# Kernel tuning notes

Measured on AMD Instinct MI355X. Metric: run time of the kernel, lower is better.

Reference implementation:

```python
import jax, jax.numpy as jnp
import numpy as np
from jax import lax

SEQ, BSZ = 64, 32
NTOK, NINP, NHID, NLAYERS = 50000, 512, 1024, 2
BN_EPS = 1e-5


def setup_inputs() -> dict:
    key = jax.random.key(0)
    ks = jax.random.split(key, 12)
    s = 0.05
    return {
        "input_ids": jax.random.randint(ks[0], (SEQ, BSZ), 0, NTOK),
        "hx": jnp.zeros((NLAYERS, BSZ, NHID), jnp.float32),
        "cx": jnp.zeros((NLAYERS, BSZ, NHID), jnp.float32),
        "emb_w": jax.random.normal(ks[1], (NTOK, NINP), jnp.float32) * 0.01,
        "Wih0": jax.random.normal(ks[2], (4 * NHID, NINP), jnp.float32) * s,
        "Whh0": jax.random.normal(ks[3], (4 * NHID, NHID), jnp.float32) * s,
        "bih0": jnp.zeros((4 * NHID,), jnp.float32),
        "bhh0": jnp.zeros((4 * NHID,), jnp.float32),
        "Wih1": jax.random.normal(ks[4], (4 * NHID, NHID), jnp.float32) * s,
        "Whh1": jax.random.normal(ks[5], (4 * NHID, NHID), jnp.float32) * s,
        "bih1": jnp.zeros((4 * NHID,), jnp.float32),
        "bhh1": jnp.zeros((4 * NHID,), jnp.float32),
        "Wp": jax.random.normal(ks[6], (NINP, NHID), jnp.float32) * s,
        "bp": jnp.zeros((NINP,), jnp.float32),
        "Wd": jax.random.normal(ks[7], (NTOK, NINP), jnp.float32) * 0.01,
        "bd": jnp.zeros((NTOK,), jnp.float32),
    }


def _lstm_cell(x, h, c, Wih, Whh, bih, bhh):
    # torch.nn.LSTMCell math; gates packed as [i, f, g, o]
    gates = x @ Wih.T + bih + h @ Whh.T + bhh  # [B, 4H]
    i, f, g, o = jnp.split(gates, 4, axis=-1)
    i = jax.nn.sigmoid(i)
    f = jax.nn.sigmoid(f)
    g = jnp.tanh(g)
    o = jax.nn.sigmoid(o)
    c2 = f * c + i * g
    h2 = o * jnp.tanh(c2)
    return h2, c2


def reference(input_ids, hx, cx, emb_w, Wih0, Whh0, bih0, bhh0,
              Wih1, Whh1, bih1, bhh1, Wp, bp, Wd, bd):
    # eval mode: drop / internal_drop / rdrop are identity; rmask == 1
    emb = emb_w[input_ids]  # [S, B, ninp]
    layers = ((Wih0, Whh0, bih0, bhh0), (Wih1, Whh1, bih1, bhh1))

    def step(carry, x_t):
        h, c = carry  # each [nlayers, B, H]
        hi = x_t
        hs, cs = [], []
        for j in range(NLAYERS):
            Wih, Whh, bih, bhh = layers[j]
            hj, cj = _lstm_cell(hi, h[j], c[j], Wih, Whh, bih, bhh)
            hs.append(hj)
            cs.append(cj)
            hi = hj
        return (jnp.stack(hs, 0), jnp.stack(cs, 0)), hi

    (hxf, cxf), out = lax.scan(step, (hx, cx), emb)  # out: [S, B, H]
    flat = out.reshape(-1, NHID)  # [S*B, H]
    # predictor: Linear -> BatchNorm1d (eval: running_mean=0, running_var=1,
    # gamma=1, beta=0) -> Tanh
    pre = flat @ Wp.T + bp
    p = jnp.tanh(pre * (1.0 / jnp.sqrt(jnp.float32(1.0 + BN_EPS))))
    decoded = p @ Wd.T + bd  # [S*B, ntoken]
    return decoded.reshape(SEQ, BSZ, NTOK), (hxf, cxf)
```

## Files before the change

### kernel.cpp

```cpp
#include <hip/hip_runtime.h>
#include <hip/hip_bf16.h>

using bf16 = __hip_bfloat16;
typedef __attribute__((ext_vector_type(8))) short short8;
typedef __attribute__((ext_vector_type(4))) float f32x4;

#define MFMA_BF16(A,B,C) __builtin_amdgcn_mfma_f32_16x16x32_bf16((A),(B),(C),0,0,0)

static __device__ __forceinline__ unsigned bf16bits(float f) {
  union { bf16 h; unsigned short u; } cv; cv.h = __float2bfloat16(f); return cv.u;
}

static __device__ __forceinline__ void gload16(const void* g, void* l) {
  __builtin_amdgcn_global_load_lds(
      (const __attribute__((address_space(1))) void*)g,
      (__attribute__((address_space(3))) void*)l, 16, 0, 0);
}

template<int EPI>
__global__ __launch_bounds__(256)
void gemm_bt(const bf16* __restrict__ A, const bf16* __restrict__ B,
             const float* __restrict__ bias1, const float* __restrict__ bias2,
             float* __restrict__ Cf, bf16* __restrict__ Cb,
             int M, int N, int K, int Nreal)
{
  __shared__ __align__(1024) bf16 As[128*32];
  __shared__ __align__(1024) bf16 Bs[128*32];
  const int tid  = threadIdx.x;
  const int wave = tid >> 6, lane = tid & 63;
  const int wr = wave >> 1, wc = wave & 1;
  const int row0 = blockIdx.y * 128;
  const int col0 = blockIdx.x * 128;

  f32x4 acc[4][4];
  #pragma unroll
  for (int m = 0; m < 4; ++m)
    #pragma unroll
    for (int n = 0; n < 4; ++n) { f32x4 z = {0.f,0.f,0.f,0.f}; acc[m][n] = z; }

  const int r_sub = lane >> 2;
  const int kc    = lane & 3;

  for (int k0 = 0; k0 < K; k0 += 32) {
    __syncthreads();
    #pragma unroll
    for (int j = 0; j < 2; ++j) {
      const int rb = wave*32 + j*16;
      gload16(A + (size_t)(row0 + rb + r_sub)*K + k0 + kc*8,
              (void*)((char*)As + (size_t)rb*64));
      gload16(B + (size_t)(col0 + rb + r_sub)*K + k0 + kc*8,
              (void*)((char*)Bs + (size_t)rb*64));
    }
    __syncthreads();

    short8 af[4], bfv[4];
    #pragma unroll
    for (int m = 0; m < 4; ++m)
      af[m] = *(const short8*)(As + (wr*64 + m*16 + (lane&15))*32 + (lane>>4)*8);
    #pragma unroll
    for (int n = 0; n < 4; ++n)
      bfv[n] = *(const short8*)(Bs + (wc*64 + n*16 + (lane&15))*32 + (lane>>4)*8);
    #pragma unroll
    for (int m = 0; m < 4; ++m)
      #pragma unroll
      for (int n = 0; n < 4; ++n)
        acc[m][n] = MFMA_BF16(af[m], bfv[n], acc[m][n]);
  }

  const float BN_SCALE = 0.9999950000374997f;
  #pragma unroll
  for (int m = 0; m < 4; ++m) {
    const int rg0 = row0 + wr*64 + m*16 + ((lane>>4)<<2);
    #pragma unroll
    for (int n = 0; n < 4; ++n) {
      const int cg = col0 + wc*64 + n*16 + (lane&15);
      if (EPI == 2) {
        const int bq = cg >> 4, q = cg & 15;
        const int orig = (q>>2)*1024 + bq*4 + (q&3);
        const float bb = bias1[orig] + bias2[orig];
        #pragma unroll
        for (int j = 0; j < 4; ++j) {
          const int row = rg0 + j;
          Cf[((size_t)bq*64 + (row>>5))*512 + (size_t)(row&31)*16 + q]
              = acc[m][n][j] + bb;
        }
      } else if (cg < Nreal) {
        float bb = 0.f;
        if (bias1) bb += bias1[cg];
        if (bias2) bb += bias2[cg];
        #pragma unroll
        for (int j = 0; j < 4; ++j) {
          float v = acc[m][n][j] + bb;
          if (EPI == 1) {
            v = tanhf(v * BN_SCALE);
            Cb[(size_t)(rg0+j)*Nreal + cg] = __float2bfloat16(v);
          } else {
            Cf[(size_t)(rg0+j)*Nreal + cg] = v;
          }
        }
      }
    }
  }
}

__global__ __launch_bounds__(256, 1)
void k_lstm_persist(const bf16* __restrict__ hinit, const float* __restrict__ cx,
                    const bf16* __restrict__ Wpack, const float* __restrict__ g0p,
                    const float* __restrict__ bih1, const float* __restrict__ bhh1,
                    bf16* __restrict__ h0_all, bf16* __restrict__ h1_all,
                    float* __restrict__ tail, unsigned* __restrict__ flags)
{
  const int b    = blockIdx.x;
  const int tid  = threadIdx.x;
  const int wave = tid >> 6, lane = tid & 63;

  __shared__ __align__(1024) bf16 Wlds[96*512];
  __shared__ float P[4][2][32][20];

  const bf16* wbase = Wpack + (size_t)b * 96 * 512;
  #pragma unroll
  for (int it = 0; it < 24; ++it) {
    const int chunk = it*4 + wave;
    gload16(wbase + (size_t)chunk*512 + lane*8,
            (void*)((char*)Wlds + (size_t)chunk*1024));
  }

  const int layer = tid >> 7;
  const int cell  = tid & 127;
  const int r     = cell >> 2;
  const int hc    = cell & 3;
  const int col   = b*4 + hc;
  float creg = cx[(size_t)layer*32768 + (size_t)r*1024 + col];
  float bsum[4];
  #pragma unroll
  for (int g = 0; g < 4; ++g)
    bsum[g] = (layer == 1) ? (bih1[g*1024 + col] + bhh1[g*1024 + col]) : 0.f;

  const int arow = lane & 15;
  const int koff = (lane >> 4) * 8;

  const unsigned* fp0 = flags + (lane*4+0)*32;
  const unsigned* fp1 = flags + (lane*4+1)*32;
  const unsigned* fp2 = flags + (lane*4+2)*32;
  const unsigned* fp3 = flags + (lane*4+3)*32;

  __syncthreads();

  for (int s = 0; s < 65; ++s) {
    const bf16* hA = (s == 0) ? hinit           : h0_all + (size_t)(s-1)*32768;
    const bf16* hB = (s <= 1) ? (hinit + 32768) : h1_all + (size_t)(s-2)*32768;

    short8 a0[8], a1[8], c0[8], c1[8];
    #pragma unroll
    for (int i = 0; i < 8; ++i) {
      const int kb = wave*256 + i*32 + koff;
      a0[i] = *(const short8*)(hA + (size_t)arow*1024      + kb);
      a1[i] = *(const short8*)(hA + (size_t)(arow+16)*1024 + kb);
      c0[i] = *(const short8*)(hB + (size_t)arow*1024      + kb);
      c1[i] = *(const short8*)(hB + (size_t)(arow+16)*1024 + kb);
    }
    float gpre[4] = {0.f, 0.f, 0.f, 0.f};
    if (layer == 0 && s < 64) {
      const float* gr = g0p + ((size_t)(b*64 + s)*32 + r)*16;
      #pragma unroll
      for (int g = 0; g < 4; ++g) gpre[g] = gr[g*4 + hc];
    }

    f32x4 z = {0.f,0.f,0.f,0.f};
    f32x4 acc00 = z, acc01 = z, acc10 = z, acc11 = z;
    #pragma unroll
    for (int i = 0; i < 8; ++i) {
      const int ks = wave*8 + i;
      short8 w0 = *(const short8*)(Wlds + ((size_t)(     ks)*64 + lane)*8);
      short8 w1 = *(const short8*)(Wlds + ((size_t)(32 + ks)*64 + lane)*8);
      short8 w2 = *(const short8*)(Wlds + ((size_t)(64 + ks)*64 + lane)*8);
      acc00 = MFMA_BF16(a0[i], w0, acc00);
      acc01 = MFMA_BF16(a1[i], w0, acc01);
      acc10 = MFMA_BF16(a0[i], w1, acc10);
      acc11 = MFMA_BF16(a1[i], w1, acc11);
      acc10 = MFMA_BF16(c0[i], w2, acc10);
      acc11 = MFMA_BF16(c1[i], w2, acc11);
    }

    #pragma unroll
    for (int j = 0; j < 4; ++j) {
      const int pr = (lane >> 4)*4 + j;
      P[wave][0][pr     ][lane & 15] = acc00[j];
      P[wave][0][pr + 16][lane & 15] = acc01[j];
      P[wave][1][pr     ][lane & 15] = acc10[j];
      P[wave][1][pr + 16][lane & 15] = acc11[j];
    }
    __syncthreads();

    const int t = s - layer;
    if (t >= 0 && t < 64) {
      float v[4];
      #pragma unroll
      for (int g = 0; g < 4; ++g) {
        const int j = g*4 + hc;
        v[g] = P[0][layer][r][j] + P[1][layer][r][j]
             + P[2][layer][r][j] + P[3][layer][r][j] + bsum[g] + gpre[g];
      }
      const float iv = 1.f/(1.f + expf(-v[0]));
      const float fv = 1.f/(1.f + expf(-v[1]));
      const float gv = tanhf(v[2]);
      const float ov = 1.f/(1.f + expf(-v[3]));
      creg = fv*creg + iv*gv;
      const float hn = ov*tanhf(creg);
      unsigned hu  = bf16bits(hn);
      unsigned p01 = hu | ((unsigned)__shfl_xor((int)hu, 1) << 16);
      unsigned p23 = (unsigned)__shfl_xor((int)p01, 2);
      if (hc == 0) {
        bf16* hp = (layer ? h1_all : h0_all) + (size_t)t*32768 + (size_t)r*1024 + b*4;
        unsigned long long v64 = (unsigned long long)p01
                               | ((unsigned long long)p23 << 32);
        __hip_atomic_store((unsigned long long*)hp, v64,
                           __ATOMIC_RELAXED, __HIP_MEMORY_SCOPE_AGENT);
      }
      if (t == 63) {
        tail[(size_t)layer*32768 + (size_t)r*1024 + col]         = hn;
        tail[65536 + (size_t)layer*32768 + (size_t)r*1024 + col] = creg;
      }
    }
    if (s == 64) break;

    __syncthreads();
    if (tid == 0) {
      asm volatile("global_store_dword %0, %1, off sc0 sc1\n\t"
                   "s_waitcnt vmcnt(0)"
                   :: "v"(flags + b*32), "v"((unsigned)(s + 1)) : "memory");
    }
    if (wave == 0) {
      const unsigned su = (unsigned)s;
      for (;;) {
        unsigned v0, v1, v2, v3;
        asm volatile("global_load_dword %0, %1, off sc0 sc1" : "=v"(v0) : "v"(fp0));
        asm volatile("global_load_dword %0, %1, off sc0 sc1" : "=v"(v1) : "v"(fp1));
        asm volatile("global_load_dword %0, %1, off sc0 sc1" : "=v"(v2) : "v"(fp2));
        asm volatile("global_load_dword %0, %1, off sc0 sc1" : "=v"(v3) : "v"(fp3));
        asm volatile("s_waitcnt vmcnt(0)" ::: "memory");
        bool ok = (v0 > su) & (v1 > su) & (v2 > su) & (v3 > su);
        if (__all(ok)) break;
        __builtin_amdgcn_s_sleep(1);
      }
    }
    __syncthreads();
    asm volatile("" ::: "memory");
    __builtin_amdgcn_sched_barrier(0);
  }
}

__global__ __launch_bounds__(256)
void k_pack(const float* __restrict__ Whh0, const float* __restrict__ Wih1,
            const float* __restrict__ Whh1, bf16* __restrict__ Wpack)
{
  const int b = blockIdx.x;
  #pragma unroll 4
  for (int it = 0; it < 24; ++it) {
    const int idx = it*256 + threadIdx.x;
    const int chunkp = idx >> 6;
    const int l = idx & 63;
    const int p = chunkp >> 5, c = chunkp & 31;
    const float* W = (p == 0) ? Whh0 : (p == 1 ? Wih1 : Whh1);
    const int j = l & 15;
    const int row = (j>>2)*1024 + b*4 + (j&3);
    const int k = c*32 + (l>>4)*8;
    const float* src = W + (size_t)row*1024 + k;
    bf16* dst = Wpack + ((size_t)(b*96 + chunkp)*64 + l)*8;
    #pragma unroll
    for (int q = 0; q < 8; ++q) dst[q] = __float2bfloat16(src[q]);
  }
}

__global__ void k_cvt(const float* __restrict__ s, bf16* __restrict__ d, long n) {
  long i = (long)blockIdx.x*blockDim.x + threadIdx.x;
  if (i < n) d[i] = __float2bfloat16(s[i]);
}

__global__ void k_cvt_perm(const float* __restrict__ src, bf16* __restrict__ dst) {
  const int n = blockIdx.x;
  const int orig = ((n>>2)&3)*1024 + (n>>4)*4 + (n&3);
  const float4 v = ((const float4*)(src + (size_t)orig*512))[threadIdx.x];
  bf16* d = dst + (size_t)n*512 + threadIdx.x*4;
  d[0] = __float2bfloat16(v.x); d[1] = __float2bfloat16(v.y);
  d[2] = __float2bfloat16(v.z); d[3] = __float2bfloat16(v.w);
}

__global__ void k_cvt_pad(const float* __restrict__ s, bf16* __restrict__ d,
                          long n, long nrows_real, int rowlen) {
  long i = (long)blockIdx.x*blockDim.x + threadIdx.x;
  if (i < n) {
    long r = i / rowlen;
    d[i] = (r < nrows_real) ? __float2bfloat16(s[i]) : __float2bfloat16(0.f);
  }
}

__global__ void k_init(const float* __restrict__ hx, bf16* __restrict__ hinit,
                       unsigned* __restrict__ flags) {
  int i = blockIdx.x*blockDim.x + threadIdx.x;
  if (i < 8192) flags[i] = 0u;
  if (i < 65536) hinit[i] = __float2bfloat16(hx[i]);
}

__global__ void k_embed(const int* __restrict__ ids, const float* __restrict__ emb_w,
                        bf16* __restrict__ out) {
  const int row = blockIdx.x;
  const int tok = ids[row];
  const float4 v = ((const float4*)(emb_w + (size_t)tok*512))[threadIdx.x];
  bf16* d = out + (size_t)row*512 + threadIdx.x*4;
  d[0] = __float2bfloat16(v.x); d[1] = __float2bfloat16(v.y);
  d[2] = __float2bfloat16(v.z); d[3] = __float2bfloat16(v.w);
}

extern "C" void kernel_launch(void* const* d_in, const int* in_sizes, int n_in,
                              void* d_out, int out_size, void* d_ws, size_t ws_size,
                              hipStream_t stream) {
  const int*   ids  = (const int*)d_in[0];
  const float* hx   = (const float*)d_in[1];
  const float* cx   = (const float*)d_in[2];
  const float* embw = (const float*)d_in[3];
  const float* Wih0 = (const float*)d_in[4];
  const float* Whh0 = (const float*)d_in[5];
  const float* bih0 = (const float*)d_in[6];
  const float* bhh0 = (const float*)d_in[7];
  const float* Wih1 = (const float*)d_in[8];
  const float* Whh1 = (const float*)d_in[9];
  const float* bih1 = (const float*)d_in[10];
  const float* bhh1 = (const float*)d_in[11];
  const float* Wp   = (const float*)d_in[12];
  const float* bp   = (const float*)d_in[13];
  const float* Wd   = (const float*)d_in[14];
  const float* bd   = (const float*)d_in[15];
  float* out = (float*)d_out;

  char* w = (char*)d_ws;
  bf16* Wih0b = (bf16*)w; w += 4096l*512*2;
  bf16* Wpack = (bf16*)w; w += 256l*96*64*8*2;
  bf16* Wpb   = (bf16*)w; w += 512l*1024*2;
  bf16* Wdb   = (bf16*)w; w += 50048l*512*2;
  bf16* embb  = (bf16*)w; w += 2048l*512*2;
  float* g0p  = (float*)w; w += 2048l*4096*4;
  bf16* h0a   = (bf16*)w; w += 2048l*1024*2;
  bf16* h1a   = (bf16*)w; w += 2048l*1024*2;
  bf16* hinit = (bf16*)w; w += 2l*32*1024*2;
  bf16* pb    = (bf16*)w; w += 2048l*512*2;
  unsigned* flags = (unsigned*)w; w += 8192*4;

  k_cvt_perm<<<4096, 128, 0, stream>>>(Wih0, Wih0b);
  k_cvt<<<(512l*1024 + 255)/256, 256, 0, stream>>>(Wp, Wpb, 512l*1024);
  k_cvt_pad<<<(50048l*512 + 255)/256, 256, 0, stream>>>(Wd, Wdb, 50048l*512, 50000, 512);
  k_init<<<256, 256, 0, stream>>>(hx, hinit, flags);
  k_embed<<<2048, 128, 0, stream>>>(ids, embw, embb);
  k_pack<<<256, 256, 0, stream>>>(Whh0, Wih1, Whh1, Wpack);

  gemm_bt<2><<<dim3(32, 16), 256, 0, stream>>>(
      embb, Wih0b, bih0, bhh0, g0p, nullptr, 2048, 4096, 512, 4096);

  float* tail = out + 102400000l;
  k_lstm_persist<<<256, 256, 0, stream>>>(hinit, cx, Wpack, g0p, bih1, bhh1,
                                          h0a, h1a, tail, flags);

  gemm_bt<1><<<dim3(4, 16), 256, 0, stream>>>(
      h1a, Wpb, bp, nullptr, nullptr, pb, 2048, 512, 1024, 512);

  gemm_bt<0><<<dim3(391, 16), 256, 0, stream>>>(
      pb, Wdb, bd, nullptr, out, nullptr, 2048, 50048, 512, 50000);
}
```

Before: 736.6 us.

## Stage decoder GEMM output through LDS for coalesced float4 stores, remap tiles

For the large decoder GEMM, the accumulator tile is staged through a shared-memory transpose buffer so each thread writes contiguous float4 chunks of output rows instead of scattered 4-byte stores. The launch is also changed to a 1D grid whose block index is remapped so consecutive blocks are spread across XCD-strided groups of tiles sharing columns of Wd. This targets write efficiency on the ~400MB logits output and L2 locality, at the cost of extra LDS usage, barriers and a 1D index computation. Since Nreal=50000 is not a multiple of 4 and rows are offset by Nreal, float4 stores at grow*Nreal may be misaligned.

```diff
diff --git a/kernel.cpp b/kernel.cpp
--- a/kernel.cpp
+++ b/kernel.cpp
@@ -26,11 +26,23 @@
 {
   __shared__ __align__(1024) bf16 As[128*32];
   __shared__ __align__(1024) bf16 Bs[128*32];
+  __shared__ float T[4][16][68];
   const int tid  = threadIdx.x;
   const int wave = tid >> 6, lane = tid & 63;
   const int wr = wave >> 1, wc = wave & 1;
-  const int row0 = blockIdx.y * 128;
-  const int col0 = blockIdx.x * 128;
+
+  int row0, col0;
+  if (EPI == 0) {
+    const int nwg  = (N >> 7) * (M >> 7);
+    const int q    = nwg >> 3;
+    const int tile = (blockIdx.x & 7) * q + (blockIdx.x >> 3);
+    const int mt   = M >> 7;
+    col0 = (tile / mt) * 128;
+    row0 = (tile % mt) * 128;
+  } else {
+    row0 = blockIdx.y * 128;
+    col0 = blockIdx.x * 128;
+  }
 
   f32x4 acc[4][4];
   #pragma unroll
@@ -68,34 +80,63 @@
   }
 
   const float BN_SCALE = 0.9999950000374997f;
-  #pragma unroll
-  for (int m = 0; m < 4; ++m) {
-    const int rg0 = row0 + wr*64 + m*16 + ((lane>>4)<<2);
-    #pragma unroll
-    for (int n = 0; n < 4; ++n) {
-      const int cg = col0 + wc*64 + n*16 + (lane&15);
-      if (EPI == 2) {
-        const int bq = cg >> 4, q = cg & 15;
-        const int orig = (q>>2)*1024 + bq*4 + (q&3);
-        const float bb = bias1[orig] + bias2[orig];
+
+  if (EPI == 0) {
+    const int rr  = lane >> 2;
+    const int cc  = (lane & 3) * 16;
+    const bool colsafe = (col0 + wc*64 + 63 < Nreal);
+    #pragma unroll
+    for (int m = 0; m < 4; ++m) {
+      __syncthreads();
+      #pragma unroll
+      for (int n = 0; n < 4; ++n) {
+        const int cg = col0 + wc*64 + n*16 + (lane&15);
+        const float bb = bias1 ? bias1[cg < Nreal ? cg : 0] : 0.f;
         #pragma unroll
-        for (int j = 0; j < 4; ++j) {
-          const int row = rg0 + j;
-          Cf[((size_t)bq*64 + (row>>5))*512 + (size_t)(row&31)*16 + q]
-              = acc[m][n][j] + bb;
+        for (int j = 0; j < 4; ++j)
+          T[wave][(lane>>4)*4 + j][n*16 + (lane&15)] = acc[m][n][j] + bb;
+      }
+      __syncthreads();
+      const int grow = row0 + wr*64 + m*16 + rr;
+      float* dst = Cf + (size_t)grow*Nreal + col0 + wc*64 + cc;
+      if (colsafe) {
+        #pragma unroll
+        for (int k = 0; k < 4; ++k)
+          *(float4*)(dst + k*4) = *(const float4*)&T[wave][rr][cc + k*4];
+      } else {
+        #pragma unroll
+        for (int k = 0; k < 16; ++k) {
+          const int cg = col0 + wc*64 + cc + k;
+          if (cg < Nreal) dst[k] = T[wave][rr][cc + k];
         }
-      } else if (cg < Nreal) {
-        float bb = 0.f;
-        if (bias1) bb += bias1[cg];
-        if (bias2) bb += bias2[cg];
-        #pragma unroll
-        for (int j = 0; j < 4; ++j) {
-          float v = acc[m][n][j] + bb;
-          if (EPI == 1) {
+      }
+    }
+  } else {
+    #pragma unroll
+    for (int m = 0; m < 4; ++m) {
+      const int rg0 = row0 + wr*64 + m*16 + ((lane>>4)<<2);
+      #pragma unroll
+      for (int n = 0; n < 4; ++n) {
+        const int cg = col0 + wc*64 + n*16 + (lane&15);
+        if (EPI == 2) {
+          const int bq = cg >> 4, q = cg & 15;
+          const int orig = (q>>2)*1024 + bq*4 + (q&3);
+          const float bb = bias1[orig] + bias2[orig];
+          #pragma unroll
+          for (int j = 0; j < 4; ++j) {
+            const int row = rg0 + j;
+            Cf[((size_t)bq*64 + (row>>5))*512 + (size_t)(row&31)*16 + q]
+                = acc[m][n][j] + bb;
+          }
+        } else if (cg < Nreal) {
+          float bb = 0.f;
+          if (bias1) bb += bias1[cg];
+          if (bias2) bb += bias2[cg];
+          #pragma unroll
+          for (int j = 0; j < 4; ++j) {
+            float v = acc[m][n][j] + bb;
             v = tanhf(v * BN_SCALE);
             Cb[(size_t)(rg0+j)*Nreal + cg] = __float2bfloat16(v);
-          } else {
-            Cf[(size_t)(rg0+j)*Nreal + cg] = v;
           }
         }
       }
@@ -363,6 +404,6 @@
   gemm_bt<1><<<dim3(4, 16), 256, 0, stream>>>(
       h1a, Wpb, bp, nullptr, nullptr, pb, 2048, 512, 1024, 512);
 
-  gemm_bt<0><<<dim3(391, 16), 256, 0, stream>>>(
+  gemm_bt<0><<<391*16, 256, 0, stream>>>(
       pb, Wdb, bd, nullptr, out, nullptr, 2048, 50048, 512, 50000);
 }
```

Result: slower. 786.6 us (+6.8%).

## Add dedicated 256x256-tile decoder GEMM kernel with 512 threads

Applied to the files above, without the earlier changes.

Replaces the generic 128x128-tile GEMM used for the large vocabulary decoder projection with a specialized kernel using 256x256 tiles, 8 waves, and direct global-to-LDS loads. The larger tile is meant to raise arithmetic intensity and cut redundant A/B reloads across the 50k-wide output. The padded decoder weight buffer grows to a multiple of 256. The generic kernel's fp32-store epilogue is removed because the decoder no longer uses it. The risks are higher register pressure (32 accumulators per lane) and a smaller grid with coarser tail waste.

```diff
diff --git a/kernel.cpp b/kernel.cpp
--- a/kernel.cpp
+++ b/kernel.cpp
@@ -91,13 +91,73 @@
         #pragma unroll
         for (int j = 0; j < 4; ++j) {
           float v = acc[m][n][j] + bb;
-          if (EPI == 1) {
-            v = tanhf(v * BN_SCALE);
-            Cb[(size_t)(rg0+j)*Nreal + cg] = __float2bfloat16(v);
-          } else {
-            Cf[(size_t)(rg0+j)*Nreal + cg] = v;
-          }
+          v = tanhf(v * BN_SCALE);
+          Cb[(size_t)(rg0+j)*Nreal + cg] = __float2bfloat16(v);
         }
+      }
+    }
+  }
+}
+
+__global__ __launch_bounds__(512, 2)
+void gemm_dec(const bf16* __restrict__ A, const bf16* __restrict__ B,
+              const float* __restrict__ bias, float* __restrict__ C,
+              int M, int N, int K, int Nreal)
+{
+  __shared__ __align__(1024) bf16 As[256*32];
+  __shared__ __align__(1024) bf16 Bs[256*32];
+  const int tid  = threadIdx.x;
+  const int wave = tid >> 6, lane = tid & 63;
+  const int wr = wave >> 2, wc = wave & 3;
+  const int row0 = blockIdx.y * 256;
+  const int col0 = blockIdx.x * 256;
+
+  f32x4 acc[8][4];
+  #pragma unroll
+  for (int m = 0; m < 8; ++m)
+    #pragma unroll
+    for (int n = 0; n < 4; ++n) { f32x4 z = {0.f,0.f,0.f,0.f}; acc[m][n] = z; }
+
+  const int r_sub = lane >> 2;
+  const int kc    = lane & 3;
+
+  for (int k0 = 0; k0 < K; k0 += 32) {
+    __syncthreads();
+    #pragma unroll
+    for (int j = 0; j < 2; ++j) {
+      const int rb = wave*32 + j*16;
+      gload16(A + (size_t)(row0 + rb + r_sub)*K + k0 + kc*8,
+              (void*)((char*)As + (size_t)rb*64));
+      gload16(B + (size_t)(col0 + rb + r_sub)*K + k0 + kc*8,
+              (void*)((char*)Bs + (size_t)rb*64));
+    }
+    __syncthreads();
+
+    short8 af[8], bfv[4];
+    #pragma unroll
+    for (int m = 0; m < 8; ++m)
+      af[m] = *(const short8*)(As + (wr*128 + m*16 + (lane&15))*32 + (lane>>4)*8);
+    #pragma unroll
+    for (int n = 0; n < 4; ++n)
+      bfv[n] = *(const short8*)(Bs + (wc*64 + n*16 + (lane&15))*32 + (lane>>4)*8);
+    #pragma unroll
+    for (int m = 0; m < 8; ++m)
+      #pragma unroll
+      for (int n = 0; n < 4; ++n)
+        acc[m][n] = MFMA_BF16(af[m], bfv[n], acc[m][n]);
+  }
+
+  #pragma unroll
+  for (int m = 0; m < 8; ++m) {
+    const int rg0 = row0 + wr*128 + m*16 + ((lane>>4)<<2);
+    #pragma unroll
+    for (int n = 0; n < 4; ++n) {
+      const int cg = col0 + wc*64 + n*16 + (lane&15);
+      if (cg < Nreal) {
+        const float bb = bias[cg];
+        #pragma unroll
+        for (int j = 0; j < 4; ++j)
+          C[(size_t)(rg0+j)*Nreal + cg] = acc[m][n][j] + bb;
       }
     }
   }
@@ -337,7 +397,7 @@
   bf16* Wih0b = (bf16*)w; w += 4096l*512*2;
   bf16* Wpack = (bf16*)w; w += 256l*96*64*8*2;
   bf16* Wpb   = (bf16*)w; w += 512l*1024*2;
-  bf16* Wdb   = (bf16*)w; w += 50048l*512*2;
+  bf16* Wdb   = (bf16*)w; w += 50176l*512*2;
   bf16* embb  = (bf16*)w; w += 2048l*512*2;
   float* g0p  = (float*)w; w += 2048l*4096*4;
   bf16* h0a   = (bf16*)w; w += 2048l*1024*2;
@@ -348,7 +408,7 @@
 
   k_cvt_perm<<<4096, 128, 0, stream>>>(Wih0, Wih0b);
   k_cvt<<<(512l*1024 + 255)/256, 256, 0, stream>>>(Wp, Wpb, 512l*1024);
-  k_cvt_pad<<<(50048l*512 + 255)/256, 256, 0, stream>>>(Wd, Wdb, 50048l*512, 50000, 512);
+  k_cvt_pad<<<(50176l*512 + 255)/256, 256, 0, stream>>>(Wd, Wdb, 50176l*512, 50000, 512);
   k_init<<<256, 256, 0, stream>>>(hx, hinit, flags);
   k_embed<<<2048, 128, 0, stream>>>(ids, embw, embb);
   k_pack<<<256, 256, 0, stream>>>(Whh0, Wih1, Whh1, Wpack);
@@ -363,6 +423,6 @@
   gemm_bt<1><<<dim3(4, 16), 256, 0, stream>>>(
       h1a, Wpb, bp, nullptr, nullptr, pb, 2048, 512, 1024, 512);
 
-  gemm_bt<0><<<dim3(391, 16), 256, 0, stream>>>(
-      pb, Wdb, bd, nullptr, out, nullptr, 2048, 50048, 512, 50000);
-}
+  gemm_dec<<<dim3(196, 8), 512, 0, stream>>>(
+      pb, Wdb, bd, out, 2048, 50176, 512, 50000);
+}
```

Result: no change. 731.8 us (-0.6%).
